# Kernel tuning notes

Measured on AMD Instinct MI355X. Metric: run time of the kernel, lower is better.

## Reference

```python
import jax, jax.numpy as jnp
import numpy as np

N = 50000          # num nodes
E = 800000         # num edges (before self loops)
DIM_IN = 128
HID = 32           # per-head hidden of conv1
HEADS = 8          # heads of conv1
DIM_OUT = 16       # output classes (conv2, 1 head, concat=False)
NEG_SLOPE = 0.2    # GATConv default leaky_relu slope


def gat_conv(x, W, a_src, a_dst, bias, src, dst, heads, out_ch, concat):
    """PyG GATConv (self-loops already appended to src/dst).
    x: [N, F_in], W: [F_in, heads*out_ch], a_src/a_dst: [heads, out_ch], bias matches output.
    """
    n = x.shape[0]
    h = (x @ W).reshape(n, heads, out_ch)                    # [N, H, C]
    al_src = jnp.einsum('nhc,hc->nh', h, a_src)              # [N, H]
    al_dst = jnp.einsum('nhc,hc->nh', h, a_dst)              # [N, H]
    e = jax.nn.leaky_relu(al_src[src] + al_dst[dst], NEG_SLOPE)   # [E', H]
    # segment softmax over edges grouped by target node (dst)
    emax = jax.ops.segment_max(e, dst, num_segments=n)       # [N, H]
    ee = jnp.exp(e - emax[dst])                              # [E', H]
    denom = jax.ops.segment_sum(ee, dst, num_segments=n)     # [N, H]
    alpha = ee / (denom[dst] + 1e-16)                        # [E', H]
    msg = h[src] * alpha[:, :, None]                         # [E', H, C]
    out = jax.ops.segment_sum(msg, dst, num_segments=n)      # [N, H, C]
    out = out.reshape(n, heads * out_ch) if concat else out.mean(axis=1)
    return out + bias


def setup_inputs() -> dict:
    key = jax.random.key(0)
    ks = jax.random.split(key, 12)
    x = jax.random.normal(ks[0], (N, DIM_IN), dtype=jnp.float32)
    edge_index = jax.random.randint(ks[1], (2, E), 0, N, dtype=jnp.int64)
    s = 0.1
    W1 = jax.random.normal(ks[2], (DIM_IN, HEADS * HID), dtype=jnp.float32) * s
    a1_src = jax.random.normal(ks[3], (HEADS, HID), dtype=jnp.float32) * s
    a1_dst = jax.random.normal(ks[4], (HEADS, HID), dtype=jnp.float32) * s
    b1 = jnp.zeros((HEADS * HID,), dtype=jnp.float32)
    W2 = jax.random.normal(ks[5], (HEADS * HID, DIM_OUT), dtype=jnp.float32) * s
    a2_src = jax.random.normal(ks[6], (1, DIM_OUT), dtype=jnp.float32) * s
    a2_dst = jax.random.normal(ks[7], (1, DIM_OUT), dtype=jnp.float32) * s
    b2 = jnp.zeros((DIM_OUT,), dtype=jnp.float32)
    return {"x": x, "edge_index": edge_index, "W1": W1, "a1_src": a1_src,
            "a1_dst": a1_dst, "b1": b1, "W2": W2, "a2_src": a2_src,
            "a2_dst": a2_dst, "b2": b2}


def reference(x, edge_index, W1, a1_src, a1_dst, b1, W2, a2_src, a2_dst, b2):
    # add self loops (GATConv default add_self_loops=True)
    loops = jnp.arange(N, dtype=edge_index.dtype)
    src = jnp.concatenate([edge_index[0], loops])
    dst = jnp.concatenate([edge_index[1], loops])
    # dropout layers are identity in eval mode
    h = gat_conv(x, W1, a1_src, a1_dst, b1, src, dst, HEADS, HID, concat=True)
    h = jax.nn.elu(h)
    out = gat_conv(h, W2, a2_src, a2_dst, b2, src, dst, 1, DIM_OUT, concat=False)
    return jax.nn.log_softmax(out, axis=1)
```

## Files before the change

### kernel.cpp

```cpp
#include <hip/hip_runtime.h>
#include <hip/hip_bf16.h>

#define NN 50000
#define EE 800000
#define EP (EE + NN)
#define DIN 128
#define HID 32
#define HEADS 8
#define C1 (HEADS * HID)
#define DOUT 16
#define NW1 3125
#define SH 9
#define NB 98
#define CAP 16384
#define EPT 8
#define BBLK (256 * EPT)

typedef __attribute__((ext_vector_type(8))) short short8;
typedef __attribute__((ext_vector_type(4))) float float4v;
typedef __attribute__((ext_vector_type(2))) float float2v;

__device__ inline unsigned short f2bf(float f) {
    __hip_bfloat16 b = __float2bfloat16(f);
    return *reinterpret_cast<unsigned short*>(&b);
}
__device__ inline float bf2f(unsigned short u) {
    union { unsigned int i; float f; } x;
    x.i = ((unsigned int)u) << 16;
    return x.f;
}
__device__ inline float bflo(unsigned u) {
    union { unsigned int i; float f; } x;
    x.i = u << 16;
    return x.f;
}
__device__ inline float bfhi(unsigned u) {
    union { unsigned int i; float f; } x;
    x.i = u & 0xffff0000u;
    return x.f;
}

__global__ __launch_bounds__(256) void k_bucketA(const int* __restrict__ ei,
                                                 int* __restrict__ cntb,
                                                 int2* __restrict__ ebuf) {
    __shared__ int hist[4][NB];
    __shared__ int base[4][NB];
    int t = threadIdx.x;
    int wave = t >> 6;
    for (int i = t; i < 4 * NB; i += 256) ((int*)hist)[i] = 0;
    __syncthreads();
    int e0 = blockIdx.x * BBLK;
    int s[EPT], d[EPT], r[EPT];
    #pragma unroll
    for (int j = 0; j < EPT; j++) {
        int e = e0 + j * 256 + t;
        int ss = 0, dd = -1;
        if (e < EE) { ss = ei[e]; dd = ei[EE + e]; }
        else if (e < EP) { ss = e - EE; dd = ss; }
        s[j] = ss; d[j] = dd;
        if (dd >= 0) r[j] = atomicAdd(&hist[wave][dd >> SH], 1);
    }
    __syncthreads();
    if (t < NB) {
        int h0 = hist[0][t], h1 = hist[1][t], h2 = hist[2][t], h3 = hist[3][t];
        int tot = h0 + h1 + h2 + h3;
        int bb = tot ? atomicAdd(&cntb[t], tot) : 0;
        base[0][t] = bb;
        base[1][t] = bb + h0;
        base[2][t] = bb + h0 + h1;
        base[3][t] = bb + h0 + h1 + h2;
    }
    __syncthreads();
    #pragma unroll
    for (int j = 0; j < EPT; j++) {
        if (d[j] >= 0) {
            int b = d[j] >> SH;
            ebuf[b * CAP + base[wave][b] + r[j]] = make_int2(s[j], d[j]);
        }
    }
}

__global__ __launch_bounds__(1024) void k_csr(const int* __restrict__ cntb,
                                              const int2* __restrict__ ebuf,
                                              int* __restrict__ row_ptr,
                                              int* __restrict__ esrc) {
    __shared__ int sdeg[512];
    __shared__ int wtot[8];
    __shared__ int bpart[2];
    int b = blockIdx.x;
    int t = threadIdx.x;
    int lane = t & 63, wave = t >> 6;
    int nodes0 = b << SH;
    if (t < 512) sdeg[t] = 0;
    if (t < 128) {
        int v = (t < b) ? cntb[t] : 0;
        #pragma unroll
        for (int off = 1; off < 64; off <<= 1) v += __shfl_xor(v, off, 64);
        if (lane == 0) bpart[wave] = v;
    }
    __syncthreads();
    int baseS = bpart[0] + bpart[1];
    int cnt = cntb[b];
    const int2* eb = ebuf + b * CAP;
    for (int i = t; i < cnt; i += 1024)
        atomicAdd(&sdeg[eb[i].y & 511], 1);
    __syncthreads();
    int v = (t < 512) ? sdeg[t] : 0;
    int inc = v;
    #pragma unroll
    for (int off = 1; off < 64; off <<= 1) {
        int u = __shfl_up(inc, off, 64);
        if (lane >= off) inc += u;
    }
    if (t < 512 && lane == 63) wtot[wave] = inc;
    __syncthreads();
    if (wave == 0 && lane < 8) {
        int w = wtot[lane];
        int iw = w;
        #pragma unroll
        for (int off = 1; off < 8; off <<= 1) {
            int u = __shfl_up(iw, off, 64);
            if (lane >= off) iw += u;
        }
        wtot[lane] = iw - w;
    }
    __syncthreads();
    int excl = inc - v + ((t < 512) ? wtot[wave] : 0);
    __syncthreads();
    if (t < 512) {
        sdeg[t] = excl;
        int node = nodes0 + t;
        if (node < NN) row_ptr[node] = baseS + excl;
    }
    __syncthreads();
    for (int i = t; i < cnt; i += 1024) {
        int2 e = eb[i];
        int pos = atomicAdd(&sdeg[e.y & 511], 1);
        esrc[baseS + pos] = e.x;
    }
    if (b == 0 && t == 0) row_ptr[NN] = EP;
}

__global__ void k_prepfw(const float* __restrict__ W1, const float* __restrict__ a1s,
                         const float* __restrict__ a1d, const float* __restrict__ W2,
                         unsigned short* __restrict__ w1frag,
                         unsigned short* __restrict__ w2frag) {
    int i = blockIdx.x * 256 + threadIdx.x;
    if (i < 17 * 2048) {
        int j = i & 7, lane = (i >> 3) & 63, s = (i >> 9) & 3, c = i >> 11;
        int q = lane >> 4, m = lane & 15;
        int k = s * 32 + q * 8 + j;
        float val;
        if (c < 16) {
            val = W1[k * C1 + c * 16 + m];
        } else {
            int h = m & 7;
            const float* av = (m < 8) ? a1s : a1d;
            float acc = 0.f;
            #pragma unroll
            for (int j2 = 0; j2 < 32; j2++)
                acc += W1[k * C1 + h * 32 + j2] * av[h * 32 + j2];
            val = acc;
        }
        w1frag[i] = f2bf(val);
    } else if (i < 17 * 2048 + 8 * 512) {
        int j2 = i - 17 * 2048;
        int jj = j2 & 7, lane = (j2 >> 3) & 63, s = j2 >> 9;
        int q = lane >> 4, m = lane & 15;
        w2frag[j2] = f2bf(W2[(s * 32 + q * 8 + jj) * DOUT + m]);
    }
}

__global__ __launch_bounds__(256) void k_gemm1(const float* __restrict__ x,
                                               const unsigned short* __restrict__ w1frag,
                                               unsigned char* __restrict__ h1f8,
                                               float* __restrict__ al1sd,
                                               unsigned short* __restrict__ al1s8) {
    int wid = (blockIdx.x * 256 + threadIdx.x) >> 6;
    int lane = threadIdx.x & 63;
    if (wid >= NW1) return;
    int nb = wid * 16;
    int m = lane & 15, quad = lane >> 4;
    const float* xrow = x + (nb + m) * DIN;

    float4 xf[8];
    #pragma unroll
    for (int s = 0; s < 4; s++) {
        xf[2 * s]     = *(const float4*)(xrow + s * 32 + quad * 8);
        xf[2 * s + 1] = *(const float4*)(xrow + s * 32 + quad * 8 + 4);
    }
    short8 bfr[4];
    #pragma unroll
    for (int s = 0; s < 4; s++) {
        unsigned short* bp = (unsigned short*)&bfr[s];
        float4 f0 = xf[2 * s], f1 = xf[2 * s + 1];
        bp[0] = f2bf(f0.x); bp[1] = f2bf(f0.y); bp[2] = f2bf(f0.z); bp[3] = f2bf(f0.w);
        bp[4] = f2bf(f1.x); bp[5] = f2bf(f1.y); bp[6] = f2bf(f1.z); bp[7] = f2bf(f1.w);
    }

    float4v acc[17];
    #pragma unroll
    for (int c = 0; c < 17; c++) acc[c] = (float4v){0.f, 0.f, 0.f, 0.f};

    #pragma unroll
    for (int s = 0; s < 4; s++) {
        const unsigned short* fp = w1frag + (s * 64 + lane) * 8;
        #pragma unroll
        for (int c = 0; c < 17; c++) {
            short8 afrag = *(const short8*)(fp + c * 2048);
            acc[c] = __builtin_amdgcn_mfma_f32_16x16x32_bf16(afrag, bfr[s], acc[c], 0, 0, 0);
        }
    }

    int node = nb + m;
    #pragma unroll
    for (int c = 0; c < 16; c++) {
        unsigned pk = 0;
        pk = __builtin_amdgcn_cvt_pk_fp8_f32(acc[c][0], acc[c][1], pk, false);
        pk = __builtin_amdgcn_cvt_pk_fp8_f32(acc[c][2], acc[c][3], pk, true);
        *(unsigned*)(h1f8 + node * C1 + c * 16 + quad * 4) = pk;
    }
    *(float4*)(al1sd + node * 16 + quad * 4) =
        make_float4(acc[16][0], acc[16][1], acc[16][2], acc[16][3]);
    if (quad < 2) {
        uint2 pk;
        pk.x = (unsigned)f2bf(acc[16][0]) | ((unsigned)f2bf(acc[16][1]) << 16);
        pk.y = (unsigned)f2bf(acc[16][2]) | ((unsigned)f2bf(acc[16][3]) << 16);
        *(uint2*)(al1s8 + node * 8 + quad * 4) = pk;
    }
}

__global__ __launch_bounds__(256) void k_agg1(const int* __restrict__ row_ptr,
                                              const int* __restrict__ esrc,
                                              const unsigned char* __restrict__ h1f8,
                                              const unsigned short* __restrict__ al1s8,
                                              const float* __restrict__ al1sd,
                                              const float* __restrict__ b1,
                                              unsigned short* __restrict__ helu_b) {
    __shared__ float wbuf[4][64 * 8];
    __shared__ int   sbuf[4][64];
    int wslot = threadIdx.x >> 6;
    int L = threadIdx.x & 63;
    int d = (blockIdx.x * 256 + threadIdx.x) >> 6;
    int h = L >> 3;
    int start = row_ptr[d], end = row_ptr[d + 1];
    float4 ald0 = *(const float4*)(al1sd + d * 16 + 8);
    float4 ald1 = *(const float4*)(al1sd + d * 16 + 12);
    float* wrow = wbuf[wslot];
    int* srow = sbuf[wslot];
    float denom = 0.f;
    float4 acc = make_float4(0.f, 0.f, 0.f, 0.f);
    const int Lofs = L * 4;

    for (int base = start; base < end; base += 64) {
        int cnt = min(64, end - base);
        int s = d;
        float wv0 = 0.f, wv1 = 0.f, wv2 = 0.f, wv3 = 0.f;
        float wv4 = 0.f, wv5 = 0.f, wv6 = 0.f, wv7 = 0.f;
        if (L < cnt) {
            s = esrc[base + L];
            uint4 as = *(const uint4*)(al1s8 + s * 8);
            float e;
            e = bflo(as.x) + ald0.x; e = e > 0.f ? e : 0.2f * e; wv0 = __expf(e);
            e = bfhi(as.x) + ald0.y; e = e > 0.f ? e : 0.2f * e; wv1 = __expf(e);
            e = bflo(as.y) + ald0.z; e = e > 0.f ? e : 0.2f * e; wv2 = __expf(e);
            e = bfhi(as.y) + ald0.w; e = e > 0.f ? e : 0.2f * e; wv3 = __expf(e);
            e = bflo(as.z) + ald1.x; e = e > 0.f ? e : 0.2f * e; wv4 = __expf(e);
            e = bfhi(as.z) + ald1.y; e = e > 0.f ? e : 0.2f * e; wv5 = __expf(e);
            e = bflo(as.w) + ald1.z; e = e > 0.f ? e : 0.2f * e; wv6 = __expf(e);
            e = bfhi(as.w) + ald1.w; e = e > 0.f ? e : 0.2f * e; wv7 = __expf(e);
        }
        srow[L] = s;
        *(float4*)&wrow[L * 8]     = make_float4(wv0, wv1, wv2, wv3);
        *(float4*)&wrow[L * 8 + 4] = make_float4(wv4, wv5, wv6, wv7);
        int cnt4 = (cnt + 3) & ~3;
        for (int i = 0; i < cnt4; i += 4) {
            int s0 = srow[i], s1 = srow[i + 1], s2 = srow[i + 2], s3 = srow[i + 3];
            float x0 = wrow[i * 8 + h];
            float x1 = wrow[i * 8 + 8 + h];
            float x2 = wrow[i * 8 + 16 + h];
            float x3 = wrow[i * 8 + 24 + h];
            unsigned v0 = *(const unsigned*)(h1f8 + s0 * C1 + Lofs);
            unsigned v1 = *(const unsigned*)(h1f8 + s1 * C1 + Lofs);
            unsigned v2 = *(const unsigned*)(h1f8 + s2 * C1 + Lofs);
            unsigned v3 = *(const unsigned*)(h1f8 + s3 * C1 + Lofs);
            denom += (x0 + x1) + (x2 + x3);
            float2v a, b;
            a = __builtin_amdgcn_cvt_pk_f32_fp8(v0, false);
            b = __builtin_amdgcn_cvt_pk_f32_fp8(v0, true);
            acc.x += x0 * a.x; acc.y += x0 * a.y; acc.z += x0 * b.x; acc.w += x0 * b.y;
            a = __builtin_amdgcn_cvt_pk_f32_fp8(v1, false);
            b = __builtin_amdgcn_cvt_pk_f32_fp8(v1, true);
            acc.x += x1 * a.x; acc.y += x1 * a.y; acc.z += x1 * b.x; acc.w += x1 * b.y;
            a = __builtin_amdgcn_cvt_pk_f32_fp8(v2, false);
            b = __builtin_amdgcn_cvt_pk_f32_fp8(v2, true);
            acc.x += x2 * a.x; acc.y += x2 * a.y; acc.z += x2 * b.x; acc.w += x2 * b.y;
            a = __builtin_amdgcn_cvt_pk_f32_fp8(v3, false);
            b = __builtin_amdgcn_cvt_pk_f32_fp8(v3, true);
            acc.x += x3 * a.x; acc.y += x3 * a.y; acc.z += x3 * b.x; acc.w += x3 * b.y;
        }
    }
    float inv = 1.0f / (denom + 1e-16f);
    float4 bv = *(const float4*)(b1 + Lofs);
    float o0 = acc.x * inv + bv.x;
    float o1 = acc.y * inv + bv.y;
    float o2 = acc.z * inv + bv.z;
    float o3 = acc.w * inv + bv.w;
    o0 = o0 > 0.f ? o0 : __expf(o0) - 1.0f;
    o1 = o1 > 0.f ? o1 : __expf(o1) - 1.0f;
    o2 = o2 > 0.f ? o2 : __expf(o2) - 1.0f;
    o3 = o3 > 0.f ? o3 : __expf(o3) - 1.0f;
    uint2 pk;
    pk.x = (unsigned)f2bf(o0) | ((unsigned)f2bf(o1) << 16);
    pk.y = (unsigned)f2bf(o2) | ((unsigned)f2bf(o3) << 16);
    *(uint2*)(helu_b + d * C1 + Lofs) = pk;
}

__global__ __launch_bounds__(256) void k_gemm2(const unsigned short* __restrict__ helu_b,
                                               const unsigned short* __restrict__ w2frag,
                                               const float* __restrict__ a2s,
                                               const float* __restrict__ a2d,
                                               unsigned short* __restrict__ h2b,
                                               float* __restrict__ al2s,
                                               float* __restrict__ al2d) {
    int wid = (blockIdx.x * 256 + threadIdx.x) >> 6;
    int lane = threadIdx.x & 63;
    int nb = wid * 16;
    if (nb >= NN) return;
    int m = lane & 15, quad = lane >> 4;

    const unsigned short* wp2 = w2frag + lane * 8;
    float4v acc = {0.f, 0.f, 0.f, 0.f};
    const unsigned short* arow = helu_b + (nb + m) * C1 + quad * 8;
    #pragma unroll
    for (int s = 0; s < 8; s++) {
        short8 afrag = *(const short8*)(arow + s * 32);
        short8 bfrag = *(const short8*)(wp2 + s * 512);
        acc = __builtin_amdgcn_mfma_f32_16x16x32_bf16(afrag, bfrag, acc, 0, 0, 0);
    }

    float as_c = a2s[m], ad_c = a2d[m];
    #pragma unroll
    for (int r = 0; r < 4; r++) {
        int node = nb + quad * 4 + r;
        float val = acc[r];
        h2b[node * DOUT + m] = f2bf(val);
        float ps = val * as_c;
        float pd = val * ad_c;
        ps += __shfl_xor(ps, 1, 64); ps += __shfl_xor(ps, 2, 64);
        ps += __shfl_xor(ps, 4, 64); ps += __shfl_xor(ps, 8, 64);
        pd += __shfl_xor(pd, 1, 64); pd += __shfl_xor(pd, 2, 64);
        pd += __shfl_xor(pd, 4, 64); pd += __shfl_xor(pd, 8, 64);
        if (m == 0) {
            al2s[node] = ps;
            al2d[node] = pd;
        }
    }
}

__global__ __launch_bounds__(256) void k_agg2(const int* __restrict__ row_ptr,
                                              const int* __restrict__ esrc,
                                              const unsigned short* __restrict__ h2b,
                                              const float* __restrict__ al2s,
                                              const float* __restrict__ al2d,
                                              const float* __restrict__ b2,
                                              float* __restrict__ out) {
    __shared__ float wbuf2[4][64];
    __shared__ int   sbuf2[4][64];
    int wslot = threadIdx.x >> 6;
    int L = threadIdx.x & 63;
    int n = (blockIdx.x * 256 + threadIdx.x) >> 6;
    if (n >= NN) return;
    int c = L & 15, g = L >> 4;
    int start = row_ptr[n], end = row_ptr[n + 1];
    float ald = al2d[n];
    float* wrow = wbuf2[wslot];
    int* srow = sbuf2[wslot];
    float acc = 0.f, denom = 0.f;

    for (int base = start; base < end; base += 64) {
        int cnt = min(64, end - base);
        int s = n; float w = 0.f;
        if (L < cnt) {
            s = esrc[base + L];
            float e = al2s[s] + ald;
            e = e > 0.f ? e : 0.2f * e;
            w = __expf(e);
        }
        srow[L] = s;
        wrow[L] = w;
        int cnt4 = (cnt + 3) & ~3;
        for (int i = 0; i < cnt4; i += 4) {
            int idx = i + g;
            int ss = srow[idx];
            float ww = wrow[idx];
            float v = bf2f(h2b[ss * DOUT + c]);
            acc += ww * v;
            denom += ww;
        }
    }
    acc += __shfl_xor(acc, 16, 64);   acc += __shfl_xor(acc, 32, 64);
    denom += __shfl_xor(denom, 16, 64); denom += __shfl_xor(denom, 32, 64);
    float val = acc / (denom + 1e-16f) + b2[c];
    float m = val;
    #pragma unroll
    for (int mm = 1; mm < 16; mm <<= 1) m = fmaxf(m, __shfl_xor(m, mm, 64));
    float ex = __expf(val - m);
    float se = ex;
    #pragma unroll
    for (int mm = 1; mm < 16; mm <<= 1) se += __shfl_xor(se, mm, 64);
    if (L < 16) out[n * DOUT + c] = val - m - __logf(se);
}

extern "C" void kernel_launch(void* const* d_in, const int* in_sizes, int n_in,
                              void* d_out, int out_size, void* d_ws, size_t ws_size,
                              hipStream_t stream) {
    const float* x   = (const float*)d_in[0];
    const int*   ei  = (const int*)d_in[1];
    const float* W1  = (const float*)d_in[2];
    const float* a1s = (const float*)d_in[3];
    const float* a1d = (const float*)d_in[4];
    const float* b1  = (const float*)d_in[5];
    const float* W2  = (const float*)d_in[6];
    const float* a2s = (const float*)d_in[7];
    const float* a2d = (const float*)d_in[8];
    const float* b2  = (const float*)d_in[9];
    float* outp = (float*)d_out;

    unsigned char* h1f8    = (unsigned char*)d_ws;
    unsigned short* helu_b = (unsigned short*)(h1f8 + NN * C1);
    unsigned short* h2b    = helu_b + NN * C1;
    unsigned short* w2frag = h2b + NN * DOUT;
    unsigned short* w1frag = w2frag + 8 * 512;
    unsigned short* al1s8  = w1frag + 17 * 2048;
    float* al1sd = (float*)(al1s8 + NN * 8);
    float* al2sb = al1sd + NN * 16;
    float* al2db = al2sb + NN;
    int* row_ptr = (int*)(al2db + NN);
    int* esrc    = row_ptr + NN + 1;
    int* cntb    = esrc + EP;
    int2* ebuf   = (int2*)helu_b;

    hipMemsetAsync(cntb, 0, NB * sizeof(int), stream);
    k_bucketA<<<(EP + BBLK - 1) / BBLK, 256, 0, stream>>>(ei, cntb, ebuf);
    k_csr<<<NB, 1024, 0, stream>>>(cntb, ebuf, row_ptr, esrc);

    k_prepfw<<<(17 * 2048 + 8 * 512 + 255) / 256, 256, 0, stream>>>(W1, a1s, a1d, W2, w1frag, w2frag);
    k_gemm1<<<(NW1 * 64 + 255) / 256, 256, 0, stream>>>(x, w1frag, h1f8, al1sd, al1s8);
    k_agg1<<<12500, 256, 0, stream>>>(row_ptr, esrc, h1f8, al1s8, al1sd, b1, helu_b);

    k_gemm2<<<(NW1 * 64 + 255) / 256, 256, 0, stream>>>(helu_b, w2frag, a2s, a2d, h2b, al2sb, al2db);
    k_agg2<<<(NN * 64 + 255) / 256, 256, 0, stream>>>(row_ptr, esrc, h2b, al2sb, al2db, b2, outp);
}
```

Baseline: 212.6 us.

## Fuse CSR build with GEMM1 and pack bucketed edges into 32-bit words

```diff
diff --git a/kernel.cpp b/kernel.cpp
--- a/kernel.cpp
+++ b/kernel.cpp
@@ -15,6 +15,7 @@
 #define CAP 16384
 #define EPT 8
 #define BBLK (256 * EPT)
+#define GB1 196
 
 typedef __attribute__((ext_vector_type(8))) short short8;
 typedef __attribute__((ext_vector_type(4))) float float4v;
@@ -23,129 +24,30 @@
 __device__ inline unsigned short f2bf(float f) {
     __hip_bfloat16 b = __float2bfloat16(f);
     return *reinterpret_cast<unsigned short*>(&b);
+}
+__device__ inline float bflo(unsigned u) {
+    union { unsigned int i; float f; } x;
+    x.i = u << 16;
+    return x.f;
+}
+__device__ inline float bfhi(unsigned u) {
+    union { unsigned int i; float f; } x;
+    x.i = u & 0xffff0000u;
+    return x.f;
 }
 __device__ inline float bf2f(unsigned short u) {
     union { unsigned int i; float f; } x;
     x.i = ((unsigned int)u) << 16;
     return x.f;
 }
-__device__ inline float bflo(unsigned u) {
-    union { unsigned int i; float f; } x;
-    x.i = u << 16;
-    return x.f;
-}
-__device__ inline float bfhi(unsigned u) {
-    union { unsigned int i; float f; } x;
-    x.i = u & 0xffff0000u;
-    return x.f;
-}
-
-__global__ __launch_bounds__(256) void k_bucketA(const int* __restrict__ ei,
-                                                 int* __restrict__ cntb,
-                                                 int2* __restrict__ ebuf) {
-    __shared__ int hist[4][NB];
-    __shared__ int base[4][NB];
-    int t = threadIdx.x;
-    int wave = t >> 6;
-    for (int i = t; i < 4 * NB; i += 256) ((int*)hist)[i] = 0;
-    __syncthreads();
-    int e0 = blockIdx.x * BBLK;
-    int s[EPT], d[EPT], r[EPT];
-    #pragma unroll
-    for (int j = 0; j < EPT; j++) {
-        int e = e0 + j * 256 + t;
-        int ss = 0, dd = -1;
-        if (e < EE) { ss = ei[e]; dd = ei[EE + e]; }
-        else if (e < EP) { ss = e - EE; dd = ss; }
-        s[j] = ss; d[j] = dd;
-        if (dd >= 0) r[j] = atomicAdd(&hist[wave][dd >> SH], 1);
-    }
-    __syncthreads();
-    if (t < NB) {
-        int h0 = hist[0][t], h1 = hist[1][t], h2 = hist[2][t], h3 = hist[3][t];
-        int tot = h0 + h1 + h2 + h3;
-        int bb = tot ? atomicAdd(&cntb[t], tot) : 0;
-        base[0][t] = bb;
-        base[1][t] = bb + h0;
-        base[2][t] = bb + h0 + h1;
-        base[3][t] = bb + h0 + h1 + h2;
-    }
-    __syncthreads();
-    #pragma unroll
-    for (int j = 0; j < EPT; j++) {
-        if (d[j] >= 0) {
-            int b = d[j] >> SH;
-            ebuf[b * CAP + base[wave][b] + r[j]] = make_int2(s[j], d[j]);
-        }
-    }
-}
-
-__global__ __launch_bounds__(1024) void k_csr(const int* __restrict__ cntb,
-                                              const int2* __restrict__ ebuf,
-                                              int* __restrict__ row_ptr,
-                                              int* __restrict__ esrc) {
-    __shared__ int sdeg[512];
-    __shared__ int wtot[8];
-    __shared__ int bpart[2];
-    int b = blockIdx.x;
-    int t = threadIdx.x;
-    int lane = t & 63, wave = t >> 6;
-    int nodes0 = b << SH;
-    if (t < 512) sdeg[t] = 0;
-    if (t < 128) {
-        int v = (t < b) ? cntb[t] : 0;
-        #pragma unroll
-        for (int off = 1; off < 64; off <<= 1) v += __shfl_xor(v, off, 64);
-        if (lane == 0) bpart[wave] = v;
-    }
-    __syncthreads();
-    int baseS = bpart[0] + bpart[1];
-    int cnt = cntb[b];
-    const int2* eb = ebuf + b * CAP;
-    for (int i = t; i < cnt; i += 1024)
-        atomicAdd(&sdeg[eb[i].y & 511], 1);
-    __syncthreads();
-    int v = (t < 512) ? sdeg[t] : 0;
-    int inc = v;
-    #pragma unroll
-    for (int off = 1; off < 64; off <<= 1) {
-        int u = __shfl_up(inc, off, 64);
-        if (lane >= off) inc += u;
-    }
-    if (t < 512 && lane == 63) wtot[wave] = inc;
-    __syncthreads();
-    if (wave == 0 && lane < 8) {
-        int w = wtot[lane];
-        int iw = w;
-        #pragma unroll
-        for (int off = 1; off < 8; off <<= 1) {
-            int u = __shfl_up(iw, off, 64);
-            if (lane >= off) iw += u;
-        }
-        wtot[lane] = iw - w;
-    }
-    __syncthreads();
-    int excl = inc - v + ((t < 512) ? wtot[wave] : 0);
-    __syncthreads();
-    if (t < 512) {
-        sdeg[t] = excl;
-        int node = nodes0 + t;
-        if (node < NN) row_ptr[node] = baseS + excl;
-    }
-    __syncthreads();
-    for (int i = t; i < cnt; i += 1024) {
-        int2 e = eb[i];
-        int pos = atomicAdd(&sdeg[e.y & 511], 1);
-        esrc[baseS + pos] = e.x;
-    }
-    if (b == 0 && t == 0) row_ptr[NN] = EP;
-}
 
 __global__ void k_prepfw(const float* __restrict__ W1, const float* __restrict__ a1s,
                          const float* __restrict__ a1d, const float* __restrict__ W2,
                          unsigned short* __restrict__ w1frag,
-                         unsigned short* __restrict__ w2frag) {
+                         unsigned short* __restrict__ w2frag,
+                         int* __restrict__ cntb) {
     int i = blockIdx.x * 256 + threadIdx.x;
+    if (blockIdx.x == 0 && threadIdx.x < NB) cntb[threadIdx.x] = 0;
     if (i < 17 * 2048) {
         int j = i & 7, lane = (i >> 3) & 63, s = (i >> 9) & 3, c = i >> 11;
         int q = lane >> 4, m = lane & 15;
@@ -171,62 +73,160 @@
     }
 }
 
-__global__ __launch_bounds__(256) void k_gemm1(const float* __restrict__ x,
-                                               const unsigned short* __restrict__ w1frag,
-                                               unsigned char* __restrict__ h1f8,
-                                               float* __restrict__ al1sd,
-                                               unsigned short* __restrict__ al1s8) {
-    int wid = (blockIdx.x * 256 + threadIdx.x) >> 6;
-    int lane = threadIdx.x & 63;
-    if (wid >= NW1) return;
-    int nb = wid * 16;
-    int m = lane & 15, quad = lane >> 4;
-    const float* xrow = x + (nb + m) * DIN;
-
-    float4 xf[8];
-    #pragma unroll
-    for (int s = 0; s < 4; s++) {
-        xf[2 * s]     = *(const float4*)(xrow + s * 32 + quad * 8);
-        xf[2 * s + 1] = *(const float4*)(xrow + s * 32 + quad * 8 + 4);
-    }
-    short8 bfr[4];
-    #pragma unroll
-    for (int s = 0; s < 4; s++) {
-        unsigned short* bp = (unsigned short*)&bfr[s];
-        float4 f0 = xf[2 * s], f1 = xf[2 * s + 1];
-        bp[0] = f2bf(f0.x); bp[1] = f2bf(f0.y); bp[2] = f2bf(f0.z); bp[3] = f2bf(f0.w);
-        bp[4] = f2bf(f1.x); bp[5] = f2bf(f1.y); bp[6] = f2bf(f1.z); bp[7] = f2bf(f1.w);
-    }
-
-    float4v acc[17];
-    #pragma unroll
-    for (int c = 0; c < 17; c++) acc[c] = (float4v){0.f, 0.f, 0.f, 0.f};
-
-    #pragma unroll
-    for (int s = 0; s < 4; s++) {
-        const unsigned short* fp = w1frag + (s * 64 + lane) * 8;
+__global__ __launch_bounds__(256) void k_bucketA(const int* __restrict__ ei,
+                                                 int* __restrict__ cntb,
+                                                 unsigned* __restrict__ ebuf) {
+    __shared__ int hist[4][NB];
+    __shared__ int base[4][NB];
+    int t = threadIdx.x;
+    int wave = t >> 6;
+    for (int i = t; i < 4 * NB; i += 256) ((int*)hist)[i] = 0;
+    __syncthreads();
+    int e0 = blockIdx.x * BBLK;
+    int s[EPT], d[EPT], r[EPT];
+    #pragma unroll
+    for (int j = 0; j < EPT; j++) {
+        int e = e0 + j * 256 + t;
+        int ss = 0, dd = -1;
+        if (e < EE) { ss = ei[e]; dd = ei[EE + e]; }
+        else if (e < EP) { ss = e - EE; dd = ss; }
+        s[j] = ss; d[j] = dd;
+        if (dd >= 0) r[j] = atomicAdd(&hist[wave][dd >> SH], 1);
+    }
+    __syncthreads();
+    if (t < NB) {
+        int h0 = hist[0][t], h1 = hist[1][t], h2 = hist[2][t], h3 = hist[3][t];
+        int tot = h0 + h1 + h2 + h3;
+        int bb = tot ? atomicAdd(&cntb[t], tot) : 0;
+        base[0][t] = bb;
+        base[1][t] = bb + h0;
+        base[2][t] = bb + h0 + h1;
+        base[3][t] = bb + h0 + h1 + h2;
+    }
+    __syncthreads();
+    #pragma unroll
+    for (int j = 0; j < EPT; j++) {
+        if (d[j] >= 0) {
+            int b = d[j] >> SH;
+            ebuf[b * CAP + base[wave][b] + r[j]] =
+                ((unsigned)s[j] << SH) | (unsigned)(d[j] & 511);
+        }
+    }
+}
+
+__global__ __launch_bounds__(1024) void k_csrgemm1(const int* __restrict__ cntb,
+                                                   const unsigned* __restrict__ ebuf,
+                                                   int* __restrict__ row_ptr,
+                                                   int* __restrict__ esrc,
+                                                   const float* __restrict__ x,
+                                                   const unsigned short* __restrict__ w1frag,
+                                                   unsigned char* __restrict__ h1f8,
+                                                   float* __restrict__ al1sd,
+                                                   unsigned short* __restrict__ al1s8) {
+    __shared__ int sdeg[512];
+    __shared__ int wtot[8];
+    __shared__ int bpart[2];
+    if (blockIdx.x < NB) {
+        int b = blockIdx.x;
+        int t = threadIdx.x;
+        int lane = t & 63, wave = t >> 6;
+        int nodes0 = b << SH;
+        if (t < 512) sdeg[t] = 0;
+        if (t < 128) {
+            int v = (t < b) ? cntb[t] : 0;
+            #pragma unroll
+            for (int off = 1; off < 64; off <<= 1) v += __shfl_xor(v, off, 64);
+            if (lane == 0) bpart[wave] = v;
+        }
+        __syncthreads();
+        int baseS = bpart[0] + bpart[1];
+        int cnt = cntb[b];
+        const unsigned* eb = ebuf + b * CAP;
+        for (int i = t; i < cnt; i += 1024)
+            atomicAdd(&sdeg[eb[i] & 511], 1);
+        __syncthreads();
+        int v = (t < 512) ? sdeg[t] : 0;
+        int inc = v;
         #pragma unroll
-        for (int c = 0; c < 17; c++) {
-            short8 afrag = *(const short8*)(fp + c * 2048);
-            acc[c] = __builtin_amdgcn_mfma_f32_16x16x32_bf16(afrag, bfr[s], acc[c], 0, 0, 0);
-        }
-    }
-
-    int node = nb + m;
-    #pragma unroll
-    for (int c = 0; c < 16; c++) {
-        unsigned pk = 0;
-        pk = __builtin_amdgcn_cvt_pk_fp8_f32(acc[c][0], acc[c][1], pk, false);
-        pk = __builtin_amdgcn_cvt_pk_fp8_f32(acc[c][2], acc[c][3], pk, true);
-        *(unsigned*)(h1f8 + node * C1 + c * 16 + quad * 4) = pk;
-    }
-    *(float4*)(al1sd + node * 16 + quad * 4) =
-        make_float4(acc[16][0], acc[16][1], acc[16][2], acc[16][3]);
-    if (quad < 2) {
-        uint2 pk;
-        pk.x = (unsigned)f2bf(acc[16][0]) | ((unsigned)f2bf(acc[16][1]) << 16);
-        pk.y = (unsigned)f2bf(acc[16][2]) | ((unsigned)f2bf(acc[16][3]) << 16);
-        *(uint2*)(al1s8 + node * 8 + quad * 4) = pk;
+        for (int off = 1; off < 64; off <<= 1) {
+            int u = __shfl_up(inc, off, 64);
+            if (lane >= off) inc += u;
+        }
+        if (t < 512 && lane == 63) wtot[wave] = inc;
+        __syncthreads();
+        if (wave == 0 && lane < 8) {
+            int w = wtot[lane];
+            int iw = w;
+            #pragma unroll
+            for (int off = 1; off < 8; off <<= 1) {
+                int u = __shfl_up(iw, off, 64);
+                if (lane >= off) iw += u;
+            }
+            wtot[lane] = iw - w;
+        }
+        __syncthreads();
+        int excl = inc - v + ((t < 512) ? wtot[wave] : 0);
+        __syncthreads();
+        if (t < 512) {
+            sdeg[t] = excl;
+            int node = nodes0 + t;
+            if (node < NN) row_ptr[node] = baseS + excl;
+        }
+        __syncthreads();
+        for (int i = t; i < cnt; i += 1024) {
+            unsigned e = eb[i];
+            int pos = atomicAdd(&sdeg[e & 511], 1);
+            esrc[baseS + pos] = (int)(e >> SH);
+        }
+        if (b == 0 && t == 0) row_ptr[NN] = EP;
+    } else {
+        int wid = (blockIdx.x - NB) * 16 + (threadIdx.x >> 6);
+        int lane = threadIdx.x & 63;
+        if (wid >= NW1) return;
+        int nb = wid * 16;
+        int m = lane & 15, quad = lane >> 4;
+        const float* xrow = x + (nb + m) * DIN;
+
+        short8 bfr[4];
+        #pragma unroll
+        for (int s = 0; s < 4; s++) {
+            float4 f0 = *(const float4*)(xrow + s * 32 + quad * 8);
+            float4 f1 = *(const float4*)(xrow + s * 32 + quad * 8 + 4);
+            unsigned short* bp = (unsigned short*)&bfr[s];
+            bp[0] = f2bf(f0.x); bp[1] = f2bf(f0.y); bp[2] = f2bf(f0.z); bp[3] = f2bf(f0.w);
+            bp[4] = f2bf(f1.x); bp[5] = f2bf(f1.y); bp[6] = f2bf(f1.z); bp[7] = f2bf(f1.w);
+        }
+
+        float4v acc[17];
+        #pragma unroll
+        for (int c = 0; c < 17; c++) acc[c] = (float4v){0.f, 0.f, 0.f, 0.f};
+
+        #pragma unroll
+        for (int s = 0; s < 4; s++) {
+            const unsigned short* fp = w1frag + (s * 64 + lane) * 8;
+            #pragma unroll
+            for (int c = 0; c < 17; c++) {
+                short8 afrag = *(const short8*)(fp + c * 2048);
+                acc[c] = __builtin_amdgcn_mfma_f32_16x16x32_bf16(afrag, bfr[s], acc[c], 0, 0, 0);
+            }
+        }
+
+        int node = nb + m;
+        #pragma unroll
+        for (int c = 0; c < 16; c++) {
+            unsigned pk = 0;
+            pk = __builtin_amdgcn_cvt_pk_fp8_f32(acc[c][0], acc[c][1], pk, false);
+            pk = __builtin_amdgcn_cvt_pk_fp8_f32(acc[c][2], acc[c][3], pk, true);
+            *(unsigned*)(h1f8 + node * C1 + c * 16 + quad * 4) = pk;
+        }
+        *(float4*)(al1sd + node * 16 + quad * 4) =
+            make_float4(acc[16][0], acc[16][1], acc[16][2], acc[16][3]);
+        if (quad < 2) {
+            uint2 pk;
+            pk.x = (unsigned)f2bf(acc[16][0]) | ((unsigned)f2bf(acc[16][1]) << 16);
+            pk.y = (unsigned)f2bf(acc[16][2]) | ((unsigned)f2bf(acc[16][3]) << 16);
+            *(uint2*)(al1s8 + node * 8 + quad * 4) = pk;
+        }
     }
 }
 
@@ -439,16 +439,13 @@
     int* row_ptr = (int*)(al2db + NN);
     int* esrc    = row_ptr + NN + 1;
     int* cntb    = esrc + EP;
-    int2* ebuf   = (int2*)helu_b;
-
-    hipMemsetAsync(cntb, 0, NB * sizeof(int), stream);
+    unsigned* ebuf = (unsigned*)helu_b;
+
+    k_prepfw<<<(17 * 2048 + 8 * 512 + 255) / 256, 256, 0, stream>>>(W1, a1s, a1d, W2, w1frag, w2frag, cntb);
     k_bucketA<<<(EP + BBLK - 1) / BBLK, 256, 0, stream>>>(ei, cntb, ebuf);
-    k_csr<<<NB, 1024, 0, stream>>>(cntb, ebuf, row_ptr, esrc);
-
-    k_prepfw<<<(17 * 2048 + 8 * 512 + 255) / 256, 256, 0, stream>>>(W1, a1s, a1d, W2, w1frag, w2frag);
-    k_gemm1<<<(NW1 * 64 + 255) / 256, 256, 0, stream>>>(x, w1frag, h1f8, al1sd, al1s8);
+    k_csrgemm1<<<NB + GB1, 1024, 0, stream>>>(cntb, ebuf, row_ptr, esrc,
+                                              x, w1frag, h1f8, al1sd, al1s8);
     k_agg1<<<12500, 256, 0, stream>>>(row_ptr, esrc, h1f8, al1s8, al1sd, b1, helu_b);
-
     k_gemm2<<<(NW1 * 64 + 255) / 256, 256, 0, stream>>>(helu_b, w2frag, a2s, a2d, h2b, al2sb, al2db);
     k_agg2<<<(NN * 64 + 255) / 256, 256, 0, stream>>>(row_ptr, esrc, h2b, al2sb, al2db, b2, outp);
 }
```

Result: no change. 215.4 us (+1.4%).
